# Performance work log

Measured on AMD Instinct MI355X. Metric: run time of the kernel, lower is better.

The kernel has to match this reference:

```python
import jax, jax.numpy as jnp
import numpy as np

N_NODES = 100000
N_EDGES = 400000
N_GRAPHS = 4000
IN_DIM = 128
HID = 512
N_DESC = 200
N_CLASSES = 2


def setup_inputs() -> dict:
    key = jax.random.key(0)
    ks = jax.random.split(key, 16)
    features = jax.random.normal(ks[0], (N_NODES, IN_DIM), jnp.float32)
    descriptors = jax.random.normal(ks[1], (N_GRAPHS, N_DESC), jnp.float32)
    src = jax.random.randint(ks[2], (N_EDGES,), 0, N_NODES)
    dst = jax.random.randint(ks[3], (N_EDGES,), 0, N_NODES)
    node2graph = jnp.sort(jax.random.randint(ks[4], (N_NODES,), 0, N_GRAPHS))

    def unif(k, shape, fan_out):
        stdv = 1.0 / np.sqrt(fan_out)
        return jax.random.uniform(k, shape, jnp.float32, -stdv, stdv)

    # GCN layer params (torch init: uniform(-1/sqrt(out), 1/sqrt(out)))
    W1 = unif(ks[5], (IN_DIM, HID), HID)
    b1 = unif(ks[6], (HID,), HID)
    W2 = unif(ks[7], (HID, HID), HID)
    b2 = unif(ks[8], (HID,), HID)
    # MLP head (torch Linear default init: uniform(-1/sqrt(fan_in), ...))
    lw1 = unif(ks[9], (HID + N_DESC, 500), HID + N_DESC)
    lb1 = unif(ks[10], (500,), HID + N_DESC)
    lw2 = unif(ks[11], (500, 100), 500)
    lb2 = unif(ks[12], (100,), 500)
    cw = unif(ks[13], (100, N_CLASSES), 100)
    cb = unif(ks[14], (N_CLASSES,), 100)
    return {"features": features, "descriptors": descriptors, "src": src,
            "dst": dst, "node2graph": node2graph, "W1": W1, "b1": b1,
            "W2": W2, "b2": b2, "lw1": lw1, "lb1": lb1, "lw2": lw2,
            "lb2": lb2, "cw": cw, "cb": cb}


def reference(features, descriptors, src, dst, node2graph,
              W1, b1, W2, b2, lw1, lb1, lw2, lb2, cw, cb):
    N = features.shape[0]
    B = descriptors.shape[0]

    def gcn(h, W, b):
        hW = h @ W                                    # [N, F_out]
        # copy_src + sum: gather source features per edge, scatter-sum to dst
        agg = jax.ops.segment_sum(hW[src], dst, num_segments=N)
        return jax.nn.relu(agg + b)

    h = gcn(features, W1, b1)                         # dropout skipped (eval)
    h = gcn(h, W2, b2)

    # dgl.mean_nodes: per-graph mean over nodes
    sums = jax.ops.segment_sum(h, node2graph, num_segments=B)     # [B, HID]
    counts = jax.ops.segment_sum(jnp.ones((N,), h.dtype), node2graph,
                                 num_segments=B)
    hg = sums / jnp.maximum(counts, 1.0)[:, None]

    x = jnp.concatenate([hg, descriptors], axis=1)    # [B, HID+N_DESC]
    x = jax.nn.relu(x @ lw1 + lb1)
    x = jax.nn.relu(x @ lw2 + lb2)
    return x @ cw + cb                                # [B, n_classes]
```

## Files before the change

### kernel.cpp

```cpp
#include <hip/hip_runtime.h>
#include <hip/hip_bf16.h>

#define N_NODES  100000
#define N_EDGES  400000
#define N_GRAPHS 4000
#define IN_DIM   128
#define HID      512
#define N_DESC   200
#define N_CLASSES 2
#define MLP1_OUT 500
#define MLP2_OUT 100
#define XIN_DIM  (HID + N_DESC)
#define XIN_PAD  768

#define SCAN_CHUNK 1024
#define NCHK ((N_NODES + SCAN_CHUNK - 1) / SCAN_CHUNK)

typedef __hip_bfloat16  bf16;
typedef __hip_bfloat162 bf16x2;
typedef short s8v  __attribute__((ext_vector_type(8)));
typedef float f32x4 __attribute__((ext_vector_type(4)));

__device__ __forceinline__ float ldf(const float* p, size_t i) { return p[i]; }
__device__ __forceinline__ float ldf(const bf16* p, size_t i)  { return __bfloat162float(p[i]); }

__device__ __forceinline__ float2 ld2(const float* p, int i) { return ((const float2*)p)[i]; }
__device__ __forceinline__ float2 ld2(const bf16* p, int i)  {
    return __bfloat1622float2(((const bf16x2*)p)[i]);
}

__device__ __forceinline__ void store_out(float* p, float v) { *p = v; }
__device__ __forceinline__ void store_out(bf16* p, float v)  { *p = __float2bfloat16(v); }

__device__ __forceinline__ short f2bs(float x) {
    bf16 h = __float2bfloat16(x);
    return __builtin_bit_cast(short, h);
}

__device__ __forceinline__ void gld16(const short* g, short* l) {
    __builtin_amdgcn_global_load_lds(
        (const __attribute__((address_space(1))) unsigned int*)g,
        (__attribute__((address_space(3))) unsigned int*)l, 16, 0, 0);
}

__global__ __launch_bounds__(256)
void detect_dtype_kernel(const unsigned* __restrict__ words, unsigned nw,
                         int* __restrict__ flag)
{
    __shared__ int s_cnt;
    if (threadIdx.x == 0) s_cnt = 0;
    __syncthreads();
    const int SAMPLES = 2048;
    int sane = 0;
    for (int i = threadIdx.x; i < SAMPLES; i += 256) {
        size_t idx = (size_t)(((unsigned long long)i * 2654435761ull) % nw);
        unsigned w = words[idx];
        float f = __uint_as_float((w & 0xFFFFu) << 16);
        float a = fabsf(f);
        if (f == 0.0f || (a > 1e-8f && a < 1e8f)) sane++;
    }
    atomicAdd(&s_cnt, sane);
    __syncthreads();
    if (threadIdx.x == 0) *flag = (s_cnt * 10 > SAMPLES * 6) ? 1 : 0;
}

template<typename FT, int MODE>
__global__ __launch_bounds__(256)
void prep_weights_kernel(const FT* __restrict__ W1, const FT* __restrict__ W2,
                         const FT* __restrict__ lw1, const FT* __restrict__ lw2,
                         const FT* __restrict__ b1, const FT* __restrict__ b2,
                         const FT* __restrict__ lb1, const FT* __restrict__ lb2,
                         short* __restrict__ W1t, short* __restrict__ W2t,
                         short* __restrict__ lw1t, short* __restrict__ lw2t,
                         float* __restrict__ b1f, float* __restrict__ b2f,
                         float* __restrict__ lb1f, float* __restrict__ lb2f,
                         const int* __restrict__ flag)
{
    if (*flag != MODE) return;
    int i = blockIdx.x * 256 + threadIdx.x;
    if (i < 65536) {
        int n = i >> 7, k = i & 127;
        W1t[i] = f2bs(ldf(W1, (size_t)k * HID + n));
        return;
    }
    i -= 65536;
    if (i < 262144) {
        int n = i >> 9, k = i & 511;
        W2t[i] = f2bs(ldf(W2, (size_t)k * HID + n));
        return;
    }
    i -= 262144;
    if (i < 393216) {
        int n = i / XIN_PAD, k = i - n * XIN_PAD;
        lw1t[i] = (n < MLP1_OUT && k < XIN_DIM)
                      ? f2bs(ldf(lw1, (size_t)k * MLP1_OUT + n)) : (short)0;
        return;
    }
    i -= 393216;
    if (i < 65536) {
        int n = i >> 9, k = i & 511;
        lw2t[i] = (n < MLP2_OUT && k < MLP1_OUT)
                      ? f2bs(ldf(lw2, (size_t)k * MLP2_OUT + n)) : (short)0;
        return;
    }
    i -= 65536;
    if (i < 512) { b1f[i] = ldf(b1, i); return; }
    i -= 512;
    if (i < 512) { b2f[i] = ldf(b2, i); return; }
    i -= 512;
    if (i < 512) { lb1f[i] = (i < MLP1_OUT) ? ldf(lb1, i) : 0.f; return; }
    i -= 512;
    if (i < 128) { lb2f[i] = (i < MLP2_OUT) ? ldf(lb2, i) : 0.f; return; }
}

__global__ __launch_bounds__(256)
void deg_kernel(const int* __restrict__ dst, int* __restrict__ deg)
{
    int e = blockIdx.x * 256 + threadIdx.x;
    if (e < N_EDGES) atomicAdd(&deg[dst[e]], 1);
}

__global__ __launch_bounds__(256)
void scan_partial_kernel(const int* __restrict__ deg, int* __restrict__ part)
{
    int c = blockIdx.x, t = threadIdx.x;
    int i0 = c * SCAN_CHUNK + t * 4;
    int s = 0;
#pragma unroll
    for (int j = 0; j < 4; j++) {
        int i = i0 + j;
        if (i < N_NODES) s += deg[i];
    }
    __shared__ int red[256];
    red[t] = s;
    __syncthreads();
    for (int off = 128; off > 0; off >>= 1) {
        if (t < off) red[t] += red[t + off];
        __syncthreads();
    }
    if (t == 0) part[c] = red[0];
}

__global__ void scan_parts_kernel(int* __restrict__ part, int* __restrict__ edge_start)
{
    int run = 0;
    for (int c = 0; c < NCHK; c++) { int v = part[c]; part[c] = run; run += v; }
    edge_start[N_NODES] = run;
}

__global__ __launch_bounds__(256)
void scan_final_kernel(const int* __restrict__ deg, const int* __restrict__ part,
                       int* __restrict__ edge_start, int* __restrict__ cursor)
{
    int c = blockIdx.x, t = threadIdx.x;
    int i0 = c * SCAN_CHUNK + t * 4;
    int d[4];
    int tsum = 0;
#pragma unroll
    for (int j = 0; j < 4; j++) {
        int i = i0 + j;
        d[j] = (i < N_NODES) ? deg[i] : 0;
        tsum += d[j];
    }
    __shared__ int s[256];
    s[t] = tsum;
    __syncthreads();
    for (int off = 1; off < 256; off <<= 1) {
        int v = (t >= off) ? s[t - off] : 0;
        __syncthreads();
        s[t] += v;
        __syncthreads();
    }
    int run = part[c] + s[t] - tsum;
#pragma unroll
    for (int j = 0; j < 4; j++) {
        int i = i0 + j;
        if (i < N_NODES) { edge_start[i] = run; cursor[i] = run; run += d[j]; }
    }
}

__global__ __launch_bounds__(256)
void fill_kernel(const int* __restrict__ src, const int* __restrict__ dst,
                 int* __restrict__ cursor, int* __restrict__ csr_src)
{
    int e = blockIdx.x * 256 + threadIdx.x;
    if (e >= N_EDGES) return;
    int p = atomicAdd(&cursor[dst[e]], 1);
    csr_src[p] = src[e];
}

__global__ __launch_bounds__(256)
void gstart_kernel(const int* __restrict__ n2g, int* __restrict__ gstart)
{
    int n = blockIdx.x * 256 + threadIdx.x;
    if (n > N_NODES) return;
    if (n == N_NODES) {
        int last = n2g[N_NODES - 1];
        for (int g = last + 1; g <= N_GRAPHS; g++) gstart[g] = N_NODES;
        return;
    }
    int v = n2g[n];
    int prev = (n == 0) ? -1 : n2g[n - 1];
    for (int g = prev + 1; g <= v; g++) gstart[g] = n;
}

template<typename FT, int MODE>
__global__ __launch_bounds__(256)
void gather_feat_kernel(const FT* __restrict__ feat, const int* __restrict__ edge_start,
                        const int* __restrict__ csr_src, bf16* __restrict__ agg1,
                        const int* __restrict__ flag)
{
    if (*flag != MODE) return;
    int n = blockIdx.x * 4 + (threadIdx.x >> 6);
    if (n >= N_NODES) return;
    int lane = threadIdx.x & 63;
    int e0 = edge_start[n], e1 = edge_start[n + 1];
    float2 acc = {0.f, 0.f};
    for (int i = e0; i < e1; i++) {
        int s = csr_src[i];
        float2 f = ld2(feat + (size_t)s * IN_DIM, lane);
        acc.x += f.x; acc.y += f.y;
    }
    bf16x2 p;
    p.x = __float2bfloat16(acc.x);
    p.y = __float2bfloat16(acc.y);
    ((bf16x2*)(agg1 + (size_t)n * IN_DIM))[lane] = p;
}

__global__ __launch_bounds__(256)
void gather_h_kernel(const bf16* __restrict__ h1, const int* __restrict__ edge_start,
                     const int* __restrict__ csr_src, bf16* __restrict__ aggc)
{
    int n = blockIdx.x * 4 + (threadIdx.x >> 6);
    if (n >= N_NODES) return;
    int lane = threadIdx.x & 63;
    int e0 = edge_start[n], e1 = edge_start[n + 1];
    float acc[8];
#pragma unroll
    for (int j = 0; j < 8; j++) acc[j] = 0.f;
    for (int i = e0; i < e1; i++) {
        int s = csr_src[i];
        float4 r = ((const float4*)(h1 + (size_t)s * HID))[lane];
        const bf16x2* p = (const bf16x2*)&r;
#pragma unroll
        for (int q = 0; q < 4; q++) {
            float2 f = __bfloat1622float2(p[q]);
            acc[2 * q] += f.x; acc[2 * q + 1] += f.y;
        }
    }
    s8v s;
#pragma unroll
    for (int j = 0; j < 8; j++) s[j] = f2bs(acc[j]);
    ((float4*)(aggc + (size_t)n * HID))[lane] = __builtin_bit_cast(float4, s);
}

template<int NCT>
__global__ __launch_bounds__(256)
void mfma_gemm_kernel(const short* __restrict__ A, const short* __restrict__ Bt,
                      const float* __restrict__ biasf, bf16* __restrict__ Cout,
                      int M, int K, int nrt)
{
    __shared__ short smem[17408];
    short* As = smem;
    short* Bs = smem + 8192;
    short* Cs = smem;

    const int b  = blockIdx.x;
    const int r8 = b & 7;
    const int t  = b >> 3;
    const int x  = (t / NCT) * 8 + r8;
    const int y  = t % NCT;
    if (x >= nrt) return;
    const int row0 = x * 128;
    const int col0 = y * 128;

    const int tid  = threadIdx.x;
    const int lane = tid & 63;
    const int w    = tid >> 6;
    const int wr = w >> 1, wc = w & 1;
    const int m  = lane & 15, q = lane >> 4;

    const int dr = lane >> 3;
    const int dc = ((lane & 7) ^ dr) * 8;
    const short* ga[4];
    const short* gb[4];
    short* la[4];
    short* lb[4];
#pragma unroll
    for (int c = 0; c < 4; c++) {
        int r = (w * 4 + c) * 8 + dr;
        ga[c] = A  + (size_t)(row0 + r) * K + dc;
        gb[c] = Bt + (size_t)(col0 + r) * K + dc;
        la[c] = As + (w * 4 + c) * 512;
        lb[c] = Bs + (w * 4 + c) * 512;
    }

    const int sa = ((q ^ (m & 7)) * 8);

    f32x4 acc[4][4];
#pragma unroll
    for (int i = 0; i < 4; i++)
#pragma unroll
        for (int j = 0; j < 4; j++) acc[i][j] = {0.f, 0.f, 0.f, 0.f};

    for (int k0 = 0; k0 < K; k0 += 64) {
#pragma unroll
        for (int c = 0; c < 4; c++) gld16(ga[c], la[c]);
#pragma unroll
        for (int c = 0; c < 4; c++) gld16(gb[c], lb[c]);
#pragma unroll
        for (int c = 0; c < 4; c++) { ga[c] += 64; gb[c] += 64; }
        __syncthreads();

#pragma unroll
        for (int kq = 0; kq < 2; kq++) {
            const int so = sa ^ (kq * 32);
            s8v av[4], bv[4];
#pragma unroll
            for (int rt = 0; rt < 4; rt++)
                av[rt] = *(const s8v*)&As[(wr * 64 + rt * 16 + m) * 64 + so];
#pragma unroll
            for (int ct = 0; ct < 4; ct++)
                bv[ct] = *(const s8v*)&Bs[(wc * 64 + ct * 16 + m) * 64 + so];
#pragma unroll
            for (int rt = 0; rt < 4; rt++)
#pragma unroll
                for (int ct = 0; ct < 4; ct++)
                    acc[rt][ct] = __builtin_amdgcn_mfma_f32_16x16x32_bf16(
                        av[rt], bv[ct], acc[rt][ct], 0, 0, 0);
        }
        __syncthreads();
    }

#pragma unroll
    for (int rt = 0; rt < 4; rt++) {
#pragma unroll
        for (int ct = 0; ct < 4; ct++) {
            int lcol = wc * 64 + ct * 16 + m;
            float bv = biasf[col0 + lcol];
#pragma unroll
            for (int reg = 0; reg < 4; reg++) {
                int lrow = wr * 64 + rt * 16 + q * 4 + reg;
                float v = acc[rt][ct][reg] + bv;
                v = v > 0.f ? v : 0.f;
                Cs[lrow * 136 + lcol] = f2bs(v);
            }
        }
    }
    __syncthreads();

#pragma unroll
    for (int it = 0; it < 8; it++) {
        int idx = it * 256 + tid;
        int r = idx >> 4;
        int c = (idx & 15) * 8;
        int row = row0 + r;
        if (row < M)
            *(float4*)&Cout[(size_t)row * HID + col0 + c] =
                *(const float4*)&Cs[r * 136 + c];
    }
}

__global__ __launch_bounds__(256)
void pool_graph_kernel(const bf16* __restrict__ h2, const int* __restrict__ gstart,
                       float* __restrict__ hg)
{
    int g = blockIdx.x * 4 + (threadIdx.x >> 6);
    if (g >= N_GRAPHS) return;
    int lane = threadIdx.x & 63;
    int s0 = gstart[g], s1 = gstart[g + 1];
    float acc[8];
#pragma unroll
    for (int j = 0; j < 8; j++) acc[j] = 0.f;
    for (int n = s0; n < s1; n++) {
        float4 r = ((const float4*)(h2 + (size_t)n * HID))[lane];
        const bf16x2* p = (const bf16x2*)&r;
#pragma unroll
        for (int q = 0; q < 4; q++) {
            float2 f = __bfloat1622float2(p[q]);
            acc[2 * q] += f.x; acc[2 * q + 1] += f.y;
        }
    }
    float* orow = hg + (size_t)g * HID + lane * 8;
    ((float4*)orow)[0] = make_float4(acc[0], acc[1], acc[2], acc[3]);
    ((float4*)orow)[1] = make_float4(acc[4], acc[5], acc[6], acc[7]);
}

template<typename FT, int MODE>
__global__ __launch_bounds__(256)
void build_xin_kernel(const float* __restrict__ hg, const int* __restrict__ gstart,
                      const FT* __restrict__ desc, bf16* __restrict__ xinb,
                      const int* __restrict__ flag)
{
    if (*flag != MODE) return;
    int idx = blockIdx.x * 256 + threadIdx.x;
    if (idx >= N_GRAPHS * XIN_PAD) return;
    int g = idx / XIN_PAD;
    int c = idx - g * XIN_PAD;
    float v;
    if (c < HID) {
        float cnt = (float)(gstart[g + 1] - gstart[g]);
        v = hg[(size_t)g * HID + c] / (cnt > 1.0f ? cnt : 1.0f);
    } else if (c < XIN_DIM) {
        v = ldf(desc, (size_t)g * N_DESC + (c - HID));
    } else {
        v = 0.f;
    }
    xinb[idx] = __float2bfloat16(v);
}

template<typename FT, int MODE>
__global__ __launch_bounds__(256)
void final_layer_kernel(const bf16* __restrict__ x2b, const FT* __restrict__ cw,
                        const FT* __restrict__ cb, FT* __restrict__ out,
                        const int* __restrict__ flag)
{
    if (*flag != MODE) return;
    int i = blockIdx.x * 256 + threadIdx.x;
    if (i >= N_GRAPHS * N_CLASSES) return;
    int r = i >> 1, c = i & 1;
    float acc = ldf(cb, c);
    const bf16* x = x2b + (size_t)r * HID;
#pragma unroll 4
    for (int k = 0; k < MLP2_OUT; k++)
        acc += __bfloat162float(x[k]) * ldf(cw, k * N_CLASSES + c);
    store_out(&out[i], acc);
}

static inline size_t align_up(size_t x, size_t a) { return (x + a - 1) & ~(a - 1); }
static inline int swgrid(int nrt, int nct) { return ((nrt + 7) / 8) * 8 * nct; }

extern "C" void kernel_launch(void* const* d_in, const int* in_sizes, int n_in,
                              void* d_out, int out_size, void* d_ws, size_t ws_size,
                              hipStream_t stream)
{
    const void* features    = d_in[0];
    const void* descriptors = d_in[1];
    const int*  src         = (const int*)d_in[2];
    const int*  dst         = (const int*)d_in[3];
    const int*  node2graph  = (const int*)d_in[4];
    const void* W1          = d_in[5];
    const void* b1          = d_in[6];
    const void* W2          = d_in[7];
    const void* b2          = d_in[8];
    const void* lw1         = d_in[9];
    const void* lb1         = d_in[10];
    const void* lw2         = d_in[11];
    const void* lb2         = d_in[12];
    const void* cw          = d_in[13];
    const void* cb          = d_in[14];
    (void)in_sizes; (void)n_in; (void)out_size; (void)ws_size;

    char* ws = (char*)d_ws;
    size_t off = 0;
    bf16* agg1 = (bf16*)(ws + off);
    bf16* aggc = (bf16*)(ws + off);
    bf16* xinb = (bf16*)(ws + off);
    bf16* x1b  = (bf16*)(ws + off + (size_t)8 * 1024 * 1024);
    bf16* x2b  = (bf16*)(ws + off + (size_t)16 * 1024 * 1024);
    off = align_up(off + (size_t)N_NODES * HID * sizeof(bf16), 256);
    bf16* h1 = (bf16*)(ws + off);
    bf16* h2 = (bf16*)(ws + off);
    off = align_up(off + (size_t)N_NODES * HID * sizeof(bf16), 256);
    float* hg = (float*)(ws + off);
    off = align_up(off + (size_t)N_GRAPHS * HID * sizeof(float), 256);
    int* dflag = (int*)(ws + off);          off = align_up(off + 256, 256);
    int* edge_start = (int*)(ws + off);     off = align_up(off + (N_NODES + 1) * 4, 256);
    int* cursor = (int*)(ws + off);         off = align_up(off + N_NODES * 4, 256);
    int* csr_src = (int*)(ws + off);        off = align_up(off + N_EDGES * 4, 256);
    int* part = (int*)(ws + off);           off = align_up(off + NCHK * 4, 256);
    int* deg = (int*)(ws + off);            off = align_up(off + N_NODES * 4, 256);
    int* gstart = (int*)(ws + off);         off = align_up(off + (N_GRAPHS + 1) * 4, 256);
    short* W1t  = (short*)(ws + off);       off = align_up(off + (size_t)HID * IN_DIM * 2, 256);
    short* W2t  = (short*)(ws + off);       off = align_up(off + (size_t)HID * HID * 2, 256);
    short* lw1t = (short*)(ws + off);       off = align_up(off + (size_t)512 * XIN_PAD * 2, 256);
    short* lw2t = (short*)(ws + off);       off = align_up(off + (size_t)128 * HID * 2, 256);
    float* b1f  = (float*)(ws + off);       off = align_up(off + 512 * 4, 256);
    float* b2f  = (float*)(ws + off);       off = align_up(off + 512 * 4, 256);
    float* lb1f = (float*)(ws + off);       off = align_up(off + 512 * 4, 256);
    float* lb2f = (float*)(ws + off);       off = align_up(off + 128 * 4, 256);

    detect_dtype_kernel<<<1, 256, 0, stream>>>(
        (const unsigned*)features, (unsigned)(N_NODES * IN_DIM / 2), dflag);

    {
        int nblk = (788096 + 255) / 256;
        prep_weights_kernel<float, 0><<<nblk, 256, 0, stream>>>(
            (const float*)W1, (const float*)W2, (const float*)lw1, (const float*)lw2,
            (const float*)b1, (const float*)b2, (const float*)lb1, (const float*)lb2,
            W1t, W2t, lw1t, lw2t, b1f, b2f, lb1f, lb2f, dflag);
        prep_weights_kernel<bf16, 1><<<nblk, 256, 0, stream>>>(
            (const bf16*)W1, (const bf16*)W2, (const bf16*)lw1, (const bf16*)lw2,
            (const bf16*)b1, (const bf16*)b2, (const bf16*)lb1, (const bf16*)lb2,
            W1t, W2t, lw1t, lw2t, b1f, b2f, lb1f, lb2f, dflag);
    }

    hipMemsetAsync(deg, 0, N_NODES * 4, stream);
    deg_kernel<<<(N_EDGES + 255) / 256, 256, 0, stream>>>(dst, deg);
    scan_partial_kernel<<<NCHK, 256, 0, stream>>>(deg, part);
    scan_parts_kernel<<<1, 1, 0, stream>>>(part, edge_start);
    scan_final_kernel<<<NCHK, 256, 0, stream>>>(deg, part, edge_start, cursor);
    fill_kernel<<<(N_EDGES + 255) / 256, 256, 0, stream>>>(src, dst, cursor, csr_src);
    gstart_kernel<<<(N_NODES + 256) / 256, 256, 0, stream>>>(node2graph, gstart);

    gather_feat_kernel<float, 0><<<N_NODES / 4, 256, 0, stream>>>(
        (const float*)features, edge_start, csr_src, agg1, dflag);
    gather_feat_kernel<bf16, 1><<<N_NODES / 4, 256, 0, stream>>>(
        (const bf16*)features, edge_start, csr_src, agg1, dflag);
    {
        int nrt = (N_NODES + 127) / 128;
        mfma_gemm_kernel<4><<<swgrid(nrt, 4), 256, 0, stream>>>(
            (const short*)agg1, W1t, b1f, h1, N_NODES, IN_DIM, nrt);
    }

    gather_h_kernel<<<N_NODES / 4, 256, 0, stream>>>(h1, edge_start, csr_src, aggc);
    {
        int nrt = (N_NODES + 127) / 128;
        mfma_gemm_kernel<4><<<swgrid(nrt, 4), 256, 0, stream>>>(
            (const short*)aggc, W2t, b2f, h2, N_NODES, HID, nrt);
    }
    pool_graph_kernel<<<N_GRAPHS / 4, 256, 0, stream>>>(h2, gstart, hg);

    {
        int nthr = (N_GRAPHS * XIN_PAD + 255) / 256;
        build_xin_kernel<float, 0><<<nthr, 256, 0, stream>>>(
            hg, gstart, (const float*)descriptors, xinb, dflag);
        build_xin_kernel<bf16, 1><<<nthr, 256, 0, stream>>>(
            hg, gstart, (const bf16*)descriptors, xinb, dflag);
    }
    {
        int nrt = (N_GRAPHS + 127) / 128;
        mfma_gemm_kernel<4><<<swgrid(nrt, 4), 256, 0, stream>>>(
            (const short*)xinb, lw1t, lb1f, x1b, N_GRAPHS, XIN_PAD, nrt);
    }
    {
        int nrt = (N_GRAPHS + 127) / 128;
        mfma_gemm_kernel<1><<<swgrid(nrt, 1), 256, 0, stream>>>(
            (const short*)x1b, lw2t, lb2f, x2b, N_GRAPHS, HID, nrt);
    }
    {
        int nthr = (N_GRAPHS * N_CLASSES + 255) / 256;
        final_layer_kernel<float, 0><<<nthr, 256, 0, stream>>>(
            x2b, (const float*)cw, (const float*)cb, (float*)d_out, dflag);
        final_layer_kernel<bf16, 1><<<nthr, 256, 0, stream>>>(
            x2b, (const bf16*)cw, (const bf16*)cb, (bf16*)d_out, dflag);
    }
}
```

Baseline: 483.6 us.

## Add 256x256-tile 8-wave MFMA GEMM with LDS double buffering for GCN layers

```diff
diff --git a/kernel.cpp b/kernel.cpp
--- a/kernel.cpp
+++ b/kernel.cpp
@@ -43,6 +43,8 @@
         (__attribute__((address_space(3))) unsigned int*)l, 16, 0, 0);
 }
 
+#define MEMFENCE asm volatile("" ::: "memory")
+
 __global__ __launch_bounds__(256)
 void detect_dtype_kernel(const unsigned* __restrict__ words, unsigned nw,
                          int* __restrict__ flag)
@@ -358,6 +360,190 @@
         if (row < M)
             *(float4*)&Cout[(size_t)row * HID + col0 + c] =
                 *(const float4*)&Cs[r * 136 + c];
+    }
+}
+
+template<int NCT>
+__global__ __launch_bounds__(512, 2)
+void mfma_gemm256_kernel(const short* __restrict__ A, const short* __restrict__ Bt,
+                         const float* __restrict__ biasf, bf16* __restrict__ Cout,
+                         int M, int K, int nrt)
+{
+    extern __shared__ short sm[];
+
+    const int b0 = blockIdx.x;
+    const int r8 = b0 & 7;
+    const int t0 = b0 >> 3;
+    const int x  = (t0 / NCT) * 8 + r8;
+    const int y  = t0 % NCT;
+    if (x >= nrt) return;
+    const int row0 = x * 256;
+    const int col0 = y * 256;
+
+    const int tid  = threadIdx.x;
+    const int lane = tid & 63;
+    const int wid  = tid >> 6;
+    const int wm   = wid >> 2;
+    const int wn   = wid & 3;
+    const int m    = lane & 15, q = lane >> 4;
+
+    const int sg0 = ((q ^ (m & 7)) << 3);
+    const int sg1 = (((4 | q) ^ (m & 7)) << 3);
+
+    const int dr8 = lane >> 3;
+    const int dg  = (((lane & 7) ^ dr8)) * 8;
+
+    const int NT = K >> 6;
+
+    const short* pA0r0 = A + (size_t)(row0 +   0 +  0 + wid * 8 + dr8) * K + dg;
+    const short* pA0r1 = A + (size_t)(row0 +   0 + 64 + wid * 8 + dr8) * K + dg;
+    const short* pA1r0 = A + (size_t)(row0 + 128 +  0 + wid * 8 + dr8) * K + dg;
+    const short* pA1r1 = A + (size_t)(row0 + 128 + 64 + wid * 8 + dr8) * K + dg;
+    const short* pB0r0 = Bt + (size_t)(col0 +   0 +  0 + wid * 8 + dr8) * K + dg;
+    const short* pB0r1 = Bt + (size_t)(col0 +   0 + 64 + wid * 8 + dr8) * K + dg;
+    const short* pB1r0 = Bt + (size_t)(col0 + 128 +  0 + wid * 8 + dr8) * K + dg;
+    const short* pB1r1 = Bt + (size_t)(col0 + 128 + 64 + wid * 8 + dr8) * K + dg;
+
+    f32x4 acc[8][4];
+#pragma unroll
+    for (int i = 0; i < 8; i++)
+#pragma unroll
+        for (int j = 0; j < 4; j++) acc[i][j] = {0.f, 0.f, 0.f, 0.f};
+
+    {
+        short* d = sm + wid * 512;
+        gld16(pA0r0, d); gld16(pA0r1, d + 4096);
+        pA0r0 += 64; pA0r1 += 64;
+        d = sm + 8192 + wid * 512;
+        gld16(pA1r0, d); gld16(pA1r1, d + 4096);
+        pA1r0 += 64; pA1r1 += 64;
+        d = sm + 16384 + wid * 512;
+        gld16(pB0r0, d); gld16(pB0r1, d + 4096);
+        pB0r0 += 64; pB0r1 += 64;
+        d = sm + 16384 + 8192 + wid * 512;
+        gld16(pB1r0, d); gld16(pB1r1, d + 4096);
+        pB1r0 += 64; pB1r1 += 64;
+        d = sm + 32768 + 16384 + wid * 512;
+        gld16(pB0r0, d); gld16(pB0r1, d + 4096);
+        pB0r0 += 64; pB0r1 += 64;
+        d = sm + 32768 + 16384 + 8192 + wid * 512;
+        gld16(pB1r0, d); gld16(pB1r1, d + 4096);
+        pB1r0 += 64; pB1r1 += 64;
+    }
+    MEMFENCE;
+    asm volatile("s_waitcnt vmcnt(4)" ::: "memory");
+    __builtin_amdgcn_s_barrier();
+    MEMFENCE;
+
+    for (int t = 0; t < NT; ++t) {
+        const int bsel = t & 1;
+        short* Ab  = sm + bsel * 32768;
+        short* Bb  = Ab + 16384;
+        short* Anx = sm + (bsel ^ 1) * 32768;
+
+        const short* a_base = Ab + (wm * 128 + m) * 64;
+        const short* b_base = Bb + (wn * 64 + m) * 64;
+
+        s8v bv[4][2];
+        s8v av[2][2];
+
+#pragma unroll
+        for (int rp = 0; rp < 4; ++rp) {
+            if (rp == 0) {
+#pragma unroll
+                for (int ct = 0; ct < 4; ++ct) {
+                    bv[ct][0] = *(const s8v*)(b_base + ct * 1024 + sg0);
+                    bv[ct][1] = *(const s8v*)(b_base + ct * 1024 + sg1);
+                }
+            }
+#pragma unroll
+            for (int i = 0; i < 2; ++i) {
+                av[i][0] = *(const s8v*)(a_base + (2 * rp + i) * 1024 + sg0);
+                av[i][1] = *(const s8v*)(a_base + (2 * rp + i) * 1024 + sg1);
+            }
+
+            if (rp == 0) {
+                if (t + 1 < NT) {
+                    short* d = Anx + wid * 512;
+                    gld16(pA0r0, d); gld16(pA0r1, d + 4096);
+                    pA0r0 += 64; pA0r1 += 64;
+                }
+            } else if (rp == 1) {
+                if (t + 1 < NT) {
+                    short* d = Anx + 8192 + wid * 512;
+                    gld16(pA1r0, d); gld16(pA1r1, d + 4096);
+                    pA1r0 += 64; pA1r1 += 64;
+                }
+            } else if (rp == 2) {
+                if (t + 2 < NT) {
+                    short* d = Bb + wid * 512;
+                    gld16(pB0r0, d); gld16(pB0r1, d + 4096);
+                    pB0r0 += 64; pB0r1 += 64;
+                }
+            } else {
+                if (t + 2 < NT) {
+                    short* d = Bb + 8192 + wid * 512;
+                    gld16(pB1r0, d); gld16(pB1r1, d + 4096);
+                    pB1r0 += 64; pB1r1 += 64;
+                }
+            }
+
+            MEMFENCE;
+            __builtin_amdgcn_s_barrier();
+            asm volatile("s_waitcnt lgkmcnt(0)" ::: "memory");
+
+            __builtin_amdgcn_s_setprio(1);
+#pragma unroll
+            for (int i = 0; i < 2; ++i)
+#pragma unroll
+                for (int ct = 0; ct < 4; ++ct)
+#pragma unroll
+                    for (int kq = 0; kq < 2; ++kq)
+                        acc[2 * rp + i][ct] = __builtin_amdgcn_mfma_f32_16x16x32_bf16(
+                            av[i][kq], bv[ct][kq], acc[2 * rp + i][ct], 0, 0, 0);
+            __builtin_amdgcn_s_setprio(0);
+
+            if (rp == 3) {
+                MEMFENCE;
+                if (t == NT - 2) asm volatile("s_waitcnt vmcnt(0)" ::: "memory");
+                else             asm volatile("s_waitcnt vmcnt(4)" ::: "memory");
+            }
+            MEMFENCE;
+            __builtin_amdgcn_s_barrier();
+            MEMFENCE;
+        }
+    }
+
+    float bias4[4];
+#pragma unroll
+    for (int ct = 0; ct < 4; ++ct) bias4[ct] = biasf[col0 + wn * 64 + ct * 16 + m];
+
+#pragma unroll
+    for (int rt = 0; rt < 8; ++rt) {
+#pragma unroll
+        for (int ct = 0; ct < 4; ++ct) {
+            const int cs = (wn * 64 + ct * 16 + m) ^ (q << 4);
+#pragma unroll
+            for (int reg = 0; reg < 4; ++reg) {
+                const int r = wm * 128 + rt * 16 + q * 4 + reg;
+                float v = acc[rt][ct][reg] + bias4[ct];
+                v = v > 0.f ? v : 0.f;
+                sm[r * 256 + cs] = f2bs(v);
+            }
+        }
+    }
+    __syncthreads();
+
+#pragma unroll
+    for (int it = 0; it < 16; ++it) {
+        int idx = it * 512 + tid;
+        int r = idx >> 5;
+        int g = idx & 31;
+        int row = row0 + r;
+        if (row < M) {
+            const float4 vv = *(const float4*)&sm[r * 256 + ((g * 8) ^ (((r >> 2) & 3) << 4))];
+            *(float4*)&Cout[(size_t)row * HID + col0 + g * 8] = vv;
+        }
     }
 }
 
@@ -450,6 +636,9 @@
     const void* cw          = d_in[13];
     const void* cb          = d_in[14];
     (void)in_sizes; (void)n_in; (void)out_size; (void)ws_size;
+
+    hipFuncSetAttribute(reinterpret_cast<const void*>(&mfma_gemm256_kernel<2>),
+                        hipFuncAttributeMaxDynamicSharedMemorySize, 131072);
 
     char* ws = (char*)d_ws;
     size_t off = 0;
@@ -508,15 +697,15 @@
     gather_feat_kernel<bf16, 1><<<N_NODES / 4, 256, 0, stream>>>(
         (const bf16*)features, edge_start, csr_src, agg1, dflag);
     {
-        int nrt = (N_NODES + 127) / 128;
-        mfma_gemm_kernel<4><<<swgrid(nrt, 4), 256, 0, stream>>>(
+        int nrt = (N_NODES + 255) / 256;
+        mfma_gemm256_kernel<2><<<swgrid(nrt, 2), 512, 131072, stream>>>(
             (const short*)agg1, W1t, b1f, h1, N_NODES, IN_DIM, nrt);
     }
 
     gather_h_kernel<<<N_NODES / 4, 256, 0, stream>>>(h1, edge_start, csr_src, aggc);
     {
-        int nrt = (N_NODES + 127) / 128;
-        mfma_gemm_kernel<4><<<swgrid(nrt, 4), 256, 0, stream>>>(
+        int nrt = (N_NODES + 255) / 256;
+        mfma_gemm256_kernel<2><<<swgrid(nrt, 2), 512, 131072, stream>>>(
             (const short*)aggc, W2t, b2f, h2, N_NODES, HID, nrt);
     }
     pool_graph_kernel<<<N_GRAPHS / 4, 256, 0, stream>>>(h2, gstart, hg);
```

Result: slower. 508.0 us (+5.0%).

## Fuse per-graph mean pooling into second GCN GEMM epilogue via atomics

Applied to the files above, without the earlier changes.

```diff
diff --git a/kernel.cpp b/kernel.cpp
--- a/kernel.cpp
+++ b/kernel.cpp
@@ -37,6 +37,10 @@
     return __builtin_bit_cast(short, h);
 }
 
+__device__ __forceinline__ float bs2f(short s) {
+    return __bfloat162float(__builtin_bit_cast(bf16, s));
+}
+
 __device__ __forceinline__ void gld16(const short* g, short* l) {
     __builtin_amdgcn_global_load_lds(
         (const __attribute__((address_space(1))) unsigned int*)g,
@@ -254,11 +258,12 @@
     ((float4*)(aggc + (size_t)n * HID))[lane] = __builtin_bit_cast(float4, s);
 }
 
-template<int NCT>
+template<int NCT, int POOL>
 __global__ __launch_bounds__(256)
 void mfma_gemm_kernel(const short* __restrict__ A, const short* __restrict__ Bt,
                       const float* __restrict__ biasf, bf16* __restrict__ Cout,
-                      int M, int K, int nrt)
+                      int M, int K, int nrt,
+                      const int* __restrict__ n2g, float* __restrict__ hg)
 {
     __shared__ short smem[17408];
     short* As = smem;
@@ -347,43 +352,44 @@
             }
         }
     }
-    __syncthreads();
-
-#pragma unroll
-    for (int it = 0; it < 8; it++) {
-        int idx = it * 256 + tid;
-        int r = idx >> 4;
-        int c = (idx & 15) * 8;
-        int row = row0 + r;
-        if (row < M)
-            *(float4*)&Cout[(size_t)row * HID + col0 + c] =
-                *(const float4*)&Cs[r * 136 + c];
-    }
-}
-
-__global__ __launch_bounds__(256)
-void pool_graph_kernel(const bf16* __restrict__ h2, const int* __restrict__ gstart,
-                       float* __restrict__ hg)
-{
-    int g = blockIdx.x * 4 + (threadIdx.x >> 6);
-    if (g >= N_GRAPHS) return;
-    int lane = threadIdx.x & 63;
-    int s0 = gstart[g], s1 = gstart[g + 1];
-    float acc[8];
-#pragma unroll
-    for (int j = 0; j < 8; j++) acc[j] = 0.f;
-    for (int n = s0; n < s1; n++) {
-        float4 r = ((const float4*)(h2 + (size_t)n * HID))[lane];
-        const bf16x2* p = (const bf16x2*)&r;
-#pragma unroll
-        for (int q = 0; q < 4; q++) {
-            float2 f = __bfloat1622float2(p[q]);
-            acc[2 * q] += f.x; acc[2 * q + 1] += f.y;
+
+    if constexpr (POOL) {
+        __shared__ int n2g_s[128];
+        if (tid < 128) {
+            int row = row0 + tid;
+            n2g_s[tid] = (row < M) ? n2g[row] : -1;
         }
-    }
-    float* orow = hg + (size_t)g * HID + lane * 8;
-    ((float4*)orow)[0] = make_float4(acc[0], acc[1], acc[2], acc[3]);
-    ((float4*)orow)[1] = make_float4(acc[4], acc[5], acc[6], acc[7]);
+        __syncthreads();
+
+        const int c = tid & 127;
+        const int h = tid >> 7;
+        float accv = 0.f;
+        int gcur = -1;
+        for (int r = h * 64; r < h * 64 + 64; ++r) {
+            int g = n2g_s[r];
+            if (g != gcur) {
+                if (gcur >= 0)
+                    atomicAdd(&hg[(size_t)gcur * HID + col0 + c], accv);
+                gcur = g;
+                accv = 0.f;
+            }
+            if (g >= 0) accv += bs2f(Cs[r * 136 + c]);
+        }
+        if (gcur >= 0)
+            atomicAdd(&hg[(size_t)gcur * HID + col0 + c], accv);
+    } else {
+        __syncthreads();
+#pragma unroll
+        for (int it = 0; it < 8; it++) {
+            int idx = it * 256 + tid;
+            int r = idx >> 4;
+            int c = (idx & 15) * 8;
+            int row = row0 + r;
+            if (row < M)
+                *(float4*)&Cout[(size_t)row * HID + col0 + c] =
+                    *(const float4*)&Cs[r * 136 + c];
+        }
+    }
 }
 
 template<typename FT, int MODE>
@@ -496,6 +502,7 @@
     }
 
     hipMemsetAsync(deg, 0, N_NODES * 4, stream);
+    hipMemsetAsync(hg, 0, (size_t)N_GRAPHS * HID * sizeof(float), stream);
     deg_kernel<<<(N_EDGES + 255) / 256, 256, 0, stream>>>(dst, deg);
     scan_partial_kernel<<<NCHK, 256, 0, stream>>>(deg, part);
     scan_parts_kernel<<<1, 1, 0, stream>>>(part, edge_start);
@@ -509,17 +516,18 @@
         (const bf16*)features, edge_start, csr_src, agg1, dflag);
     {
         int nrt = (N_NODES + 127) / 128;
-        mfma_gemm_kernel<4><<<swgrid(nrt, 4), 256, 0, stream>>>(
-            (const short*)agg1, W1t, b1f, h1, N_NODES, IN_DIM, nrt);
+        mfma_gemm_kernel<4, 0><<<swgrid(nrt, 4), 256, 0, stream>>>(
+            (const short*)agg1, W1t, b1f, h1, N_NODES, IN_DIM, nrt,
+            nullptr, nullptr);
     }
 
     gather_h_kernel<<<N_NODES / 4, 256, 0, stream>>>(h1, edge_start, csr_src, aggc);
     {
         int nrt = (N_NODES + 127) / 128;
-        mfma_gemm_kernel<4><<<swgrid(nrt, 4), 256, 0, stream>>>(
-            (const short*)aggc, W2t, b2f, h2, N_NODES, HID, nrt);
-    }
-    pool_graph_kernel<<<N_GRAPHS / 4, 256, 0, stream>>>(h2, gstart, hg);
+        mfma_gemm_kernel<4, 1><<<swgrid(nrt, 4), 256, 0, stream>>>(
+            (const short*)aggc, W2t, b2f, h2, N_NODES, HID, nrt,
+            node2graph, hg);
+    }
 
     {
         int nthr = (N_GRAPHS * XIN_PAD + 255) / 256;
@@ -530,13 +538,15 @@
     }
     {
         int nrt = (N_GRAPHS + 127) / 128;
-        mfma_gemm_kernel<4><<<swgrid(nrt, 4), 256, 0, stream>>>(
-            (const short*)xinb, lw1t, lb1f, x1b, N_GRAPHS, XIN_PAD, nrt);
+        mfma_gemm_kernel<4, 0><<<swgrid(nrt, 4), 256, 0, stream>>>(
+            (const short*)xinb, lw1t, lb1f, x1b, N_GRAPHS, XIN_PAD, nrt,
+            nullptr, nullptr);
     }
     {
         int nrt = (N_GRAPHS + 127) / 128;
-        mfma_gemm_kernel<1><<<swgrid(nrt, 1), 256, 0, stream>>>(
-            (const short*)x1b, lw2t, lb2f, x2b, N_GRAPHS, HID, nrt);
+        mfma_gemm_kernel<1, 0><<<swgrid(nrt, 1), 256, 0, stream>>>(
+            (const short*)x1b, lw2t, lb2f, x2b, N_GRAPHS, HID, nrt,
+            nullptr, nullptr);
     }
     {
         int nthr = (N_GRAPHS * N_CLASSES + 255) / 256;
```

Measured after the change: 492.6 us. About the same (+1.8%).
